# Kernel tuning notes

Measured on AMD Instinct MI355X. Metric: run time of the kernel, lower is better.

Reference implementation:

```python
import jax, jax.numpy as jnp
import numpy as np

N = 50000      # nodes
E = 640000     # edges
HID = 64       # hid_dim (per-head channels C)
HEADS = 4
D = HID * HEADS  # 256, conv output dim (concat=True)
LN_EPS = 1e-5


def setup_inputs() -> dict:
    key = jax.random.key(0)
    ks = jax.random.split(key, 10)
    def w(k, shape, scale=0.05):
        return jax.random.normal(k, shape, dtype=jnp.float32) * scale
    x = jax.random.normal(ks[0], (N, HID), dtype=jnp.float32)
    edge_index = jax.random.randint(ks[1], (2, E), 0, N)
    return {
        'x': x,
        'edge_index': edge_index,
        'Wq': w(ks[2], (D, HID)), 'bq': jnp.zeros((D,), jnp.float32),
        'Wk': w(ks[3], (D, HID)), 'bk': jnp.zeros((D,), jnp.float32),
        'Wv': w(ks[4], (D, HID)), 'bv': jnp.zeros((D,), jnp.float32),
        'Wskip': w(ks[5], (D, HID)), 'bskip': jnp.zeros((D,), jnp.float32),
        'Wbeta': w(ks[6], (1, 3 * D)),
        'ln_g': jnp.ones((D,), jnp.float32), 'ln_b': jnp.zeros((D,), jnp.float32),
        'Wproj': w(ks[7], (HID, D)), 'bproj': jnp.zeros((HID,), jnp.float32),
    }


def _layer(x, edge_index, Wq, bq, Wk, bk, Wv, bv, Wskip, bskip, Wbeta, ln_g, ln_b, Wproj, bproj):
    src, dst = edge_index[0], edge_index[1]  # message flows src -> dst
    # q/k/v projections, [N, H, C]
    q = (x @ Wq.T + bq).reshape(N, HEADS, HID)
    k = (x @ Wk.T + bk).reshape(N, HEADS, HID)
    v = (x @ Wv.T + bv).reshape(N, HEADS, HID)
    # edge-wise attention logits: [E, H]
    alpha = jnp.einsum('ehc,ehc->eh', q[dst], k[src]) / jnp.sqrt(jnp.float32(HID))
    # per-destination-node softmax (segment softmax)
    m = jax.ops.segment_max(alpha, dst, num_segments=N)          # [N, H]
    ex = jnp.exp(alpha - m[dst])                                 # [E, H]
    s = jax.ops.segment_sum(ex, dst, num_segments=N)             # [N, H]
    attn = ex / (s[dst] + 1e-16)                                 # [E, H]
    # weighted scatter-aggregate of values -> [N, H*C]
    msg = (v[src] * attn[..., None]).reshape(E, D)
    out = jax.ops.segment_sum(msg, dst, num_segments=N)          # [N, D]
    # beta gated skip (TransformerConv beta=True, root_weight=True)
    x_r = x @ Wskip.T + bskip                                    # [N, D]
    beta = jax.nn.sigmoid(jnp.concatenate([out, x_r, out - x_r], axis=-1) @ Wbeta.T)  # [N, 1]
    h = beta * x_r + (1.0 - beta) * out
    # LayerNorm over last dim
    mu = jnp.mean(h, axis=-1, keepdims=True)
    var = jnp.var(h, axis=-1, keepdims=True)
    h = (h - mu) * jax.lax.rsqrt(var + LN_EPS) * ln_g + ln_b
    # projection + residual + ReLU (dropout = identity in eval)
    h = h @ Wproj.T + bproj
    return jax.nn.relu(h + x)


def reference(x, edge_index, Wq, bq, Wk, bk, Wv, bv, Wskip, bskip, Wbeta, ln_g, ln_b, Wproj, bproj):
    return _layer(x, edge_index, Wq, bq, Wk, bk, Wv, bv, Wskip, bskip, Wbeta, ln_g, ln_b, Wproj, bproj)
```

## Files before the change

### kernel.cpp

```cpp
#include <hip/hip_runtime.h>
#include <stdint.h>

#define NND 50000
#define NED 640000

typedef unsigned short u16;
typedef unsigned int u32;
typedef __attribute__((ext_vector_type(8))) short short8;
typedef __attribute__((ext_vector_type(4))) float f32x4;
typedef __attribute__((ext_vector_type(2))) float fx2;

__device__ __forceinline__ float bf2f(u16 u) {
    union { u32 i; float f; } x; x.i = ((u32)u) << 16; return x.f;
}
__device__ __forceinline__ u16 f2bf(float f) {
    union { u32 i; float f; } x; x.f = f;
    u32 u = x.i;
    return (u16)((u + 0x7fffu + ((u >> 16) & 1u)) >> 16);
}
__device__ __forceinline__ float bflo(u32 w) {
    union { u32 i; float f; } x; x.i = w << 16; return x.f;
}
__device__ __forceinline__ float bfhi(u32 w) {
    union { u32 i; float f; } x; x.i = w & 0xffff0000u; return x.f;
}
__device__ __forceinline__ u32 pk2(float lo, float hi) {
    return (u32)f2bf(lo) | ((u32)f2bf(hi) << 16);
}
__device__ __forceinline__ u32 pk_fp8_4(u32 w0, u32 w1) {
    u32 p = __builtin_amdgcn_cvt_pk_fp8_f32(bflo(w0), bfhi(w0), 0, false);
    p = __builtin_amdgcn_cvt_pk_fp8_f32(bflo(w1), bfhi(w1), p, true);
    return p;
}
__device__ __forceinline__ void dec8v(u32 a, u32 b, fx2* f) {
    f[0] = __builtin_amdgcn_cvt_pk_f32_fp8(a, false);
    f[1] = __builtin_amdgcn_cvt_pk_f32_fp8(a, true);
    f[2] = __builtin_amdgcn_cvt_pk_f32_fp8(b, false);
    f[3] = __builtin_amdgcn_cvt_pk_f32_fp8(b, true);
}

__global__ void k_wt(const float* __restrict__ Wq, const float* __restrict__ Wk,
                     const float* __restrict__ Wv, const float* __restrict__ Ws,
                     const float* __restrict__ Wp,
                     const float* __restrict__ bq, const float* __restrict__ bk,
                     const float* __restrict__ bv, const float* __restrict__ bs,
                     u16* __restrict__ wb, float* __restrict__ bias_c,
                     u16* __restrict__ wpA) {
    int idx = blockIdx.x * 256 + threadIdx.x;
    if (idx < 65536) {
        int j = idx & 7;
        int lane = (idx >> 3) & 63;
        int q = (idx >> 9) & 1;
        int dt = idx >> 10;
        int dim = dt * 16 + (lane & 15);
        int k = q * 32 + ((lane >> 4) & 3) * 8 + j;
        int mat = dim >> 8, r = dim & 255;
        const float* W = (mat == 0) ? Wq : (mat == 1) ? Wk : (mat == 2) ? Wv : Ws;
        float v = W[r * 64 + k] * ((mat == 0) ? 0.125f : 1.0f);
        wb[idx] = f2bf(v);
    } else if (idx < 65536 + 1024) {
        int dim = idx - 65536;
        int mat = dim >> 8, r = dim & 255;
        const float* B = (mat == 0) ? bq : (mat == 1) ? bk : (mat == 2) ? bv : bs;
        bias_c[dim] = B[r] * ((mat == 0) ? 0.125f : 1.0f);
    } else if (idx < 65536 + 1024 + 16384) {
        int w = idx - 66560;
        int j = w & 7;
        int lane = (w >> 3) & 63;
        int kc = (w >> 9) & 7;
        int mt = w >> 12;
        int dim = mt * 16 + (lane & 15);
        int k = kc * 32 + ((lane >> 4) & 3) * 8 + j;
        wpA[w] = f2bf(Wp[dim * 256 + k]);
    }
}

#define CNT_BLKS 2500
#define PPAD 1040
__global__ __launch_bounds__(256) void k_fillproj(
    const int* __restrict__ esrc, const int* __restrict__ edst,
    int* __restrict__ deg, int* __restrict__ csr,
    const float* __restrict__ x, const u16* __restrict__ wb,
    const float* __restrict__ bias_c,
    uint2* __restrict__ q8, uint4* __restrict__ kv8, u16* __restrict__ xr16)
{
    __shared__ u16 hb[16 * PPAD];
    if (blockIdx.x < CNT_BLKS) {
        int e = blockIdx.x * 256 + threadIdx.x;
        if (e < NED) {
            int d = edst[e];
            int pos = atomicAdd(&deg[d], 1);
            if (pos < 64) csr[(d << 6) + pos] = esrc[e];
        }
        return;
    }
    const int t = threadIdx.x;
    const int wave = t >> 6, lane = t & 63;
    const int node0 = (blockIdx.x - CNT_BLKS) * 16;
    const int lr = lane & 15, quad = lane >> 4;

    int node = node0 + lr;
    if (node > NND - 1) node = NND - 1;
    short8 xf0, xf1;
    {
        const float* xp = x + (size_t)node * 64 + quad * 8;
        float4 a = *reinterpret_cast<const float4*>(xp);
        float4 b = *reinterpret_cast<const float4*>(xp + 4);
        float4 c = *reinterpret_cast<const float4*>(xp + 32);
        float4 d = *reinterpret_cast<const float4*>(xp + 36);
        xf0[0] = (short)f2bf(a.x); xf0[1] = (short)f2bf(a.y);
        xf0[2] = (short)f2bf(a.z); xf0[3] = (short)f2bf(a.w);
        xf0[4] = (short)f2bf(b.x); xf0[5] = (short)f2bf(b.y);
        xf0[6] = (short)f2bf(b.z); xf0[7] = (short)f2bf(b.w);
        xf1[0] = (short)f2bf(c.x); xf1[1] = (short)f2bf(c.y);
        xf1[2] = (short)f2bf(c.z); xf1[3] = (short)f2bf(c.w);
        xf1[4] = (short)f2bf(d.x); xf1[5] = (short)f2bf(d.y);
        xf1[6] = (short)f2bf(d.z); xf1[7] = (short)f2bf(d.w);
    }
    #pragma unroll 4
    for (int dtl = 0; dtl < 16; ++dtl) {
        int dt = wave * 16 + dtl;
        const u16* wp = wb + (size_t)(dt * 2) * 512 + lane * 8;
        short8 a0 = *reinterpret_cast<const short8*>(wp);
        short8 a1 = *reinterpret_cast<const short8*>(wp + 512);
        f32x4 bias = *reinterpret_cast<const f32x4*>(bias_c + dt * 16 + quad * 4);
        f32x4 acc = {0.f, 0.f, 0.f, 0.f};
        acc = __builtin_amdgcn_mfma_f32_16x16x32_bf16(a0, xf0, acc, 0, 0, 0);
        acc = __builtin_amdgcn_mfma_f32_16x16x32_bf16(a1, xf1, acc, 0, 0, 0);
        uint2 st;
        st.x = pk2(acc[0] + bias[0], acc[1] + bias[1]);
        st.y = pk2(acc[2] + bias[2], acc[3] + bias[3]);
        *reinterpret_cast<uint2*>(&hb[lr * PPAD + dt * 16 + quad * 4]) = st;
    }
    __syncthreads();
    #pragma unroll
    for (int it = 0; it < 2; ++it) {
        int idx = it * 256 + t;
        int nip = idx >> 5, g = idx & 31;
        int gnode = node0 + nip;
        if (gnode < NND) {
            const u16* hp = &hb[nip * PPAD];
            *reinterpret_cast<uint4*>(xr16 + (size_t)gnode * 256 + g * 8) =
                *reinterpret_cast<const uint4*>(hp + 768 + g * 8);
            uint4 qw = *reinterpret_cast<const uint4*>(hp + g * 8);
            uint2 qs;
            qs.x = pk_fp8_4(qw.x, qw.y);
            qs.y = pk_fp8_4(qw.z, qw.w);
            q8[(size_t)gnode * 32 + g] = qs;
            uint4 kw = *reinterpret_cast<const uint4*>(hp + 256 + g * 8);
            uint4 vw = *reinterpret_cast<const uint4*>(hp + 512 + g * 8);
            uint4 kvs;
            kvs.x = pk_fp8_4(kw.x, kw.y);
            kvs.y = pk_fp8_4(kw.z, kw.w);
            kvs.z = pk_fp8_4(vw.x, vw.y);
            kvs.w = pk_fp8_4(vw.z, vw.w);
            kv8[(size_t)gnode * 32 + g] = kvs;
        }
    }
}

#define PS 264
__global__ __launch_bounds__(256) void k_attnepi(
    const int* __restrict__ deg, const int* __restrict__ csr,
    const uint2* __restrict__ q8, const uint4* __restrict__ kv8,
    const u16* __restrict__ xr16, const float* __restrict__ x,
    const float* __restrict__ Wbeta, const float* __restrict__ ln_g,
    const float* __restrict__ ln_b, const u16* __restrict__ wpA,
    const float* __restrict__ bproj, float* __restrict__ y)
{
    __shared__ u16 hn[16 * PS];
    const int t = threadIdx.x;
    const int wave = t >> 6, lane = t & 63;
    const int l32 = lane & 31, half = lane >> 5;
    const int lr = lane & 15, grp = lane >> 4;
    const int base = blockIdx.x * 16;

    for (int nt = 0; nt < 4; ++nt) {
        int lid = wave * 4 + nt;
        int node = base + lid;
        if (node >= NND) break;
        uint2 qv = q8[(size_t)node * 32 + l32];
        fx2 q[4];
        dec8v(qv.x, qv.y, q);
        int dg = __builtin_amdgcn_readfirstlane(deg[node]);
        if (dg > 64) dg = 64;
        int r0 = node << 6;
        int r1 = r0 + dg;
        float s = 0.f;
        fx2 acc0 = {0.f, 0.f}, acc1 = {0.f, 0.f}, acc2 = {0.f, 0.f}, acc3 = {0.f, 0.f};
        int i = r0;
        for (; i + 8 <= r1; i += 8) {
            int c0 = csr[i + 0], c1 = csr[i + 1], c2 = csr[i + 2], c3 = csr[i + 3];
            int c4 = csr[i + 4], c5 = csr[i + 5], c6 = csr[i + 6], c7 = csr[i + 7];
            int e0 = half ? c4 : c0;
            int e1 = half ? c5 : c1;
            int e2 = half ? c6 : c2;
            int e3 = half ? c7 : c3;
            uint4 kv0 = kv8[(size_t)e0 * 32 + l32];
            uint4 kv1 = kv8[(size_t)e1 * 32 + l32];
            uint4 kv2 = kv8[(size_t)e2 * 32 + l32];
            uint4 kv3 = kv8[(size_t)e3 * 32 + l32];
            fx2 k0[4], k1[4], k2[4], k3[4];
            dec8v(kv0.x, kv0.y, k0); dec8v(kv1.x, kv1.y, k1);
            dec8v(kv2.x, kv2.y, k2); dec8v(kv3.x, kv3.y, k3);
            fx2 t0 = q[0]*k0[0] + q[1]*k0[1] + q[2]*k0[2] + q[3]*k0[3];
            fx2 t1 = q[0]*k1[0] + q[1]*k1[1] + q[2]*k1[2] + q[3]*k1[3];
            fx2 t2 = q[0]*k2[0] + q[1]*k2[1] + q[2]*k2[2] + q[3]*k2[3];
            fx2 t3 = q[0]*k3[0] + q[1]*k3[1] + q[2]*k3[2] + q[3]*k3[3];
            float pa = t0.x + t0.y, pb = t1.x + t1.y, pc = t2.x + t2.y, pd = t3.x + t3.y;
            pa += __shfl_xor(pa, 1); pa += __shfl_xor(pa, 2); pa += __shfl_xor(pa, 4);
            pb += __shfl_xor(pb, 1); pb += __shfl_xor(pb, 2); pb += __shfl_xor(pb, 4);
            pc += __shfl_xor(pc, 1); pc += __shfl_xor(pc, 2); pc += __shfl_xor(pc, 4);
            pd += __shfl_xor(pd, 1); pd += __shfl_xor(pd, 2); pd += __shfl_xor(pd, 4);
            float ea = __expf(pa), eb = __expf(pb), ec = __expf(pc), ed = __expf(pd);
            s += (ea + eb) + (ec + ed);
            fx2 ev0 = {ea, ea}, ev1 = {eb, eb}, ev2 = {ec, ec}, ev3 = {ed, ed};
            fx2 v0[4], v1[4], v2[4], v3[4];
            dec8v(kv0.z, kv0.w, v0); dec8v(kv1.z, kv1.w, v1);
            dec8v(kv2.z, kv2.w, v2); dec8v(kv3.z, kv3.w, v3);
            acc0 = acc0 + ev0*v0[0] + ev1*v1[0] + ev2*v2[0] + ev3*v3[0];
            acc1 = acc1 + ev0*v0[1] + ev1*v1[1] + ev2*v2[1] + ev3*v3[1];
            acc2 = acc2 + ev0*v0[2] + ev1*v1[2] + ev2*v2[2] + ev3*v3[2];
            acc3 = acc3 + ev0*v0[3] + ev1*v1[3] + ev2*v2[3] + ev3*v3[3];
        }
        for (; i + 4 <= r1; i += 4) {
            int c0 = csr[i + 0], c1 = csr[i + 1], c2 = csr[i + 2], c3 = csr[i + 3];
            int e0 = half ? c2 : c0;
            int e1 = half ? c3 : c1;
            uint4 kv0 = kv8[(size_t)e0 * 32 + l32];
            uint4 kv1 = kv8[(size_t)e1 * 32 + l32];
            fx2 k0[4], k1[4];
            dec8v(kv0.x, kv0.y, k0); dec8v(kv1.x, kv1.y, k1);
            fx2 t0 = q[0]*k0[0] + q[1]*k0[1] + q[2]*k0[2] + q[3]*k0[3];
            fx2 t1 = q[0]*k1[0] + q[1]*k1[1] + q[2]*k1[2] + q[3]*k1[3];
            float pa = t0.x + t0.y, pb = t1.x + t1.y;
            pa += __shfl_xor(pa, 1); pa += __shfl_xor(pa, 2); pa += __shfl_xor(pa, 4);
            pb += __shfl_xor(pb, 1); pb += __shfl_xor(pb, 2); pb += __shfl_xor(pb, 4);
            float ea = __expf(pa), eb = __expf(pb);
            s += ea + eb;
            fx2 ev0 = {ea, ea}, ev1 = {eb, eb};
            fx2 v0[4], v1[4];
            dec8v(kv0.z, kv0.w, v0); dec8v(kv1.z, kv1.w, v1);
            acc0 = acc0 + ev0*v0[0] + ev1*v1[0];
            acc1 = acc1 + ev0*v0[1] + ev1*v1[1];
            acc2 = acc2 + ev0*v0[2] + ev1*v1[2];
            acc3 = acc3 + ev0*v0[3] + ev1*v1[3];
        }
        for (; i < r1; i += 2) {
            int ii = i + half;
            bool valid = ii < r1;
            if (ii > r1 - 1) ii = r1 - 1;
            int e0 = csr[ii];
            uint4 kv0 = kv8[(size_t)e0 * 32 + l32];
            fx2 k0[4];
            dec8v(kv0.x, kv0.y, k0);
            fx2 t0 = q[0]*k0[0] + q[1]*k0[1] + q[2]*k0[2] + q[3]*k0[3];
            float pa = t0.x + t0.y;
            pa += __shfl_xor(pa, 1); pa += __shfl_xor(pa, 2); pa += __shfl_xor(pa, 4);
            float ea = valid ? __expf(pa) : 0.f;
            s += ea;
            fx2 ev0 = {ea, ea};
            fx2 v0[4];
            dec8v(kv0.z, kv0.w, v0);
            acc0 = acc0 + ev0*v0[0];
            acc1 = acc1 + ev0*v0[1];
            acc2 = acc2 + ev0*v0[2];
            acc3 = acc3 + ev0*v0[3];
        }
        float a0 = acc0.x, a1 = acc0.y, a2 = acc1.x, a3 = acc1.y;
        float a4 = acc2.x, a5 = acc2.y, a6 = acc3.x, a7 = acc3.y;
        s  += __shfl_xor(s, 32);
        a0 += __shfl_xor(a0, 32); a1 += __shfl_xor(a1, 32);
        a2 += __shfl_xor(a2, 32); a3 += __shfl_xor(a3, 32);
        a4 += __shfl_xor(a4, 32); a5 += __shfl_xor(a5, 32);
        a6 += __shfl_xor(a6, 32); a7 += __shfl_xor(a7, 32);
        float inv = 1.0f / (s + 1e-16f);
        if (half == 0) {
            uint4 st;
            st.x = pk2(a0 * inv, a1 * inv);
            st.y = pk2(a2 * inv, a3 * inv);
            st.z = pk2(a4 * inv, a5 * inv);
            st.w = pk2(a6 * inv, a7 * inv);
            *reinterpret_cast<uint4*>(&hn[lid * PS + l32 * 8]) = st;
        }
    }
    __syncthreads();

    {
        const float4* wb4 = reinterpret_cast<const float4*>(Wbeta);
        const float4* g44 = reinterpret_cast<const float4*>(ln_g);
        const float4* b44 = reinterpret_cast<const float4*>(ln_b);
        float wo[16], wx[16], wd[16], gg[16], bb[16];
        #pragma unroll
        for (int j = 0; j < 4; ++j) {
            float4 a = wb4[lr * 4 + j];
            float4 b = wb4[64 + lr * 4 + j];
            float4 c = wb4[128 + lr * 4 + j];
            float4 g = g44[lr * 4 + j];
            float4 bl = b44[lr * 4 + j];
            wo[j*4+0]=a.x; wo[j*4+1]=a.y; wo[j*4+2]=a.z; wo[j*4+3]=a.w;
            wx[j*4+0]=b.x; wx[j*4+1]=b.y; wx[j*4+2]=b.z; wx[j*4+3]=b.w;
            wd[j*4+0]=c.x; wd[j*4+1]=c.y; wd[j*4+2]=c.z; wd[j*4+3]=c.w;
            gg[j*4+0]=g.x; gg[j*4+1]=g.y; gg[j*4+2]=g.z; gg[j*4+3]=g.w;
            bb[j*4+0]=bl.x; bb[j*4+1]=bl.y; bb[j*4+2]=bl.z; bb[j*4+3]=bl.w;
        }
        int lid = wave * 4 + grp;
        int node = base + lid;
        if (node < NND) {
            uint4 u0 = *reinterpret_cast<const uint4*>(&hn[lid * PS + lr * 16]);
            uint4 u1 = *reinterpret_cast<const uint4*>(&hn[lid * PS + lr * 16 + 8]);
            const uint4* xp = reinterpret_cast<const uint4*>(xr16 + (size_t)node * 256 + lr * 16);
            uint4 v0 = xp[0], v1 = xp[1];
            float o[16], r[16];
            o[0]=bflo(u0.x); o[1]=bfhi(u0.x); o[2]=bflo(u0.y); o[3]=bfhi(u0.y);
            o[4]=bflo(u0.z); o[5]=bfhi(u0.z); o[6]=bflo(u0.w); o[7]=bfhi(u0.w);
            o[8]=bflo(u1.x); o[9]=bfhi(u1.x); o[10]=bflo(u1.y); o[11]=bfhi(u1.y);
            o[12]=bflo(u1.z); o[13]=bfhi(u1.z); o[14]=bflo(u1.w); o[15]=bfhi(u1.w);
            r[0]=bflo(v0.x); r[1]=bfhi(v0.x); r[2]=bflo(v0.y); r[3]=bfhi(v0.y);
            r[4]=bflo(v0.z); r[5]=bfhi(v0.z); r[6]=bflo(v0.w); r[7]=bfhi(v0.w);
            r[8]=bflo(v1.x); r[9]=bfhi(v1.x); r[10]=bflo(v1.y); r[11]=bfhi(v1.y);
            r[12]=bflo(v1.z); r[13]=bfhi(v1.z); r[14]=bflo(v1.w); r[15]=bfhi(v1.w);
            float part = 0.f;
            #pragma unroll
            for (int cc = 0; cc < 16; ++cc)
                part = fmaf(wo[cc], o[cc], fmaf(wx[cc], r[cc], fmaf(wd[cc], o[cc]-r[cc], part)));
            part += __shfl_xor(part, 1); part += __shfl_xor(part, 2);
            part += __shfl_xor(part, 4); part += __shfl_xor(part, 8);
            float beta = 1.0f / (1.0f + __expf(-part));
            float h[16];
            float sh = 0.f, sq = 0.f;
            #pragma unroll
            for (int cc = 0; cc < 16; ++cc) {
                h[cc] = beta * r[cc] + (1.f - beta) * o[cc];
                sh += h[cc];
                sq = fmaf(h[cc], h[cc], sq);
            }
            sh += __shfl_xor(sh, 1); sh += __shfl_xor(sh, 2);
            sh += __shfl_xor(sh, 4); sh += __shfl_xor(sh, 8);
            sq += __shfl_xor(sq, 1); sq += __shfl_xor(sq, 2);
            sq += __shfl_xor(sq, 4); sq += __shfl_xor(sq, 8);
            float mu = sh * (1.0f / 256.0f);
            float var = sq * (1.0f / 256.0f) - mu * mu;
            float ri = rsqrtf(var + 1e-5f);
            u32 pw[8];
            #pragma unroll
            for (int pp = 0; pp < 8; ++pp) {
                float z0 = (h[pp*2+0] - mu) * ri * gg[pp*2+0] + bb[pp*2+0];
                float z1 = (h[pp*2+1] - mu) * ri * gg[pp*2+1] + bb[pp*2+1];
                pw[pp] = pk2(z0, z1);
            }
            uint4 s0, s1;
            s0.x = pw[0]; s0.y = pw[1]; s0.z = pw[2]; s0.w = pw[3];
            s1.x = pw[4]; s1.y = pw[5]; s1.z = pw[6]; s1.w = pw[7];
            *reinterpret_cast<uint4*>(&hn[lid * PS + lr * 16]) = s0;
            *reinterpret_cast<uint4*>(&hn[lid * PS + lr * 16 + 8]) = s1;
        }
    }
    __syncthreads();

    {
        const int mt = wave;
        f32x4 acc = {0.f, 0.f, 0.f, 0.f};
        #pragma unroll
        for (int kc = 0; kc < 8; ++kc) {
            short8 a = *reinterpret_cast<const short8*>(wpA + ((size_t)(mt * 8 + kc) * 64 + lane) * 8);
            short8 b = *reinterpret_cast<const short8*>(&hn[lr * PS + kc * 32 + grp * 8]);
            acc = __builtin_amdgcn_mfma_f32_16x16x32_bf16(a, b, acc, 0, 0, 0);
        }
        int node = base + lr;
        if (node < NND) {
            int d0 = mt * 16 + grp * 4;
            float4 bp4 = *reinterpret_cast<const float4*>(bproj + d0);
            float4 xv = *reinterpret_cast<const float4*>(x + (size_t)node * 64 + d0);
            float4 rr;
            rr.x = fmaxf(acc[0] + bp4.x + xv.x, 0.f);
            rr.y = fmaxf(acc[1] + bp4.y + xv.y, 0.f);
            rr.z = fmaxf(acc[2] + bp4.z + xv.z, 0.f);
            rr.w = fmaxf(acc[3] + bp4.w + xv.w, 0.f);
            *reinterpret_cast<float4*>(y + (size_t)node * 64 + d0) = rr;
        }
    }
}

extern "C" void kernel_launch(void* const* d_in, const int* in_sizes, int n_in,
                              void* d_out, int out_size, void* d_ws, size_t ws_size,
                              hipStream_t stream) {
    const float* x     = (const float*)d_in[0];
    const int*   eidx  = (const int*)d_in[1];
    const float* Wq    = (const float*)d_in[2];
    const float* bq    = (const float*)d_in[3];
    const float* Wk    = (const float*)d_in[4];
    const float* bk    = (const float*)d_in[5];
    const float* Wv    = (const float*)d_in[6];
    const float* bv    = (const float*)d_in[7];
    const float* Wsk   = (const float*)d_in[8];
    const float* bsk   = (const float*)d_in[9];
    const float* Wbeta = (const float*)d_in[10];
    const float* lng   = (const float*)d_in[11];
    const float* lnb   = (const float*)d_in[12];
    const float* Wp    = (const float*)d_in[13];
    const float* bp    = (const float*)d_in[14];
    float* y = (float*)d_out;

    char* ws = (char*)d_ws;
    size_t off = 0;
    auto alloc = [&](size_t b) { size_t o = off; off += (b + 255) & ~(size_t)255; return o; };
    uint2* q8   = (uint2*)(ws + alloc((size_t)NND * 256));
    uint4* kv8  = (uint4*)(ws + alloc((size_t)NND * 512));
    u16*  xr16  = (u16*)(ws + alloc((size_t)NND * 512));
    int* deg    = (int*)(ws + alloc((size_t)NND * 4));
    int* csr    = (int*)(ws + alloc((size_t)NND * 64 * 4));
    u16* wb     = (u16*)(ws + alloc((size_t)65536 * 2));
    float* bias_c = (float*)(ws + alloc((size_t)1024 * 4));
    u16* wpA    = (u16*)(ws + alloc((size_t)16384 * 2));

    hipMemsetAsync(deg, 0, (size_t)NND * 4, stream);
    k_wt      <<<324, 256, 0, stream>>>(Wq, Wk, Wv, Wsk, Wp, bq, bk, bv, bsk,
                                        wb, bias_c, wpA);
    k_fillproj<<<CNT_BLKS + (NND + 15) / 16, 256, 0, stream>>>(
                 eidx, eidx + NED, deg, csr, x, wb, bias_c, q8, kv8, xr16);
    k_attnepi <<<(NND + 15) / 16, 256, 0, stream>>>(deg, csr, q8, kv8, xr16, x,
                                                    Wbeta, lng, lnb, wpA, bp, y);
}
```

Before: 238.4 us.

## Prefetch kv gathers, vectorize csr loads, 32 nodes per block, fold deg memset

The attention kernel now software-pipelines its gather loop: it loads the next 8 neighbours' CSR indices (as int4) and kv rows before processing the current batch, so memory latency overlaps compute. Each block handles 32 nodes instead of 16, and the epilogue and MFMA projection loop twice per wave, which spreads weight loads over more nodes. The deg memset moves into the weight-prep kernel, removing one launch. The prefetch registers and larger LDS footprint raise register and shared-memory pressure, which may reduce occupancy.

New measurement: 241.4 us. Within noise of the previous version (+1.2%).

```diff
diff --git a/kernel.cpp b/kernel.cpp
--- a/kernel.cpp
+++ b/kernel.cpp
@@ -45,7 +45,7 @@
                      const float* __restrict__ bq, const float* __restrict__ bk,
                      const float* __restrict__ bv, const float* __restrict__ bs,
                      u16* __restrict__ wb, float* __restrict__ bias_c,
-                     u16* __restrict__ wpA) {
+                     u16* __restrict__ wpA, int* __restrict__ deg) {
     int idx = blockIdx.x * 256 + threadIdx.x;
     if (idx < 65536) {
         int j = idx & 7;
@@ -72,6 +72,8 @@
         int dim = mt * 16 + (lane & 15);
         int k = kc * 32 + ((lane >> 4) & 3) * 8 + j;
         wpA[w] = f2bf(Wp[dim * 256 + k]);
+    } else if (idx < 65536 + 1024 + 16384 + NND) {
+        deg[idx - 82944] = 0;
     }
 }
 
@@ -160,6 +162,7 @@
 }
 
 #define PS 264
+#define NPB 32
 __global__ __launch_bounds__(256) void k_attnepi(
     const int* __restrict__ deg, const int* __restrict__ csr,
     const uint2* __restrict__ q8, const uint4* __restrict__ kv8,
@@ -168,15 +171,16 @@
     const float* __restrict__ ln_b, const u16* __restrict__ wpA,
     const float* __restrict__ bproj, float* __restrict__ y)
 {
-    __shared__ u16 hn[16 * PS];
+    __shared__ u16 hn[NPB * PS];
     const int t = threadIdx.x;
-    const int wave = t >> 6, lane = t & 63;
+    const int wave = __builtin_amdgcn_readfirstlane(t >> 6);
+    const int lane = t & 63;
     const int l32 = lane & 31, half = lane >> 5;
     const int lr = lane & 15, grp = lane >> 4;
-    const int base = blockIdx.x * 16;
-
-    for (int nt = 0; nt < 4; ++nt) {
-        int lid = wave * 4 + nt;
+    const int base = blockIdx.x * NPB;
+
+    for (int nt = 0; nt < 8; ++nt) {
+        int lid = wave * 8 + nt;
         int node = base + lid;
         if (node >= NND) break;
         uint2 qv = q8[(size_t)node * 32 + l32];
@@ -188,21 +192,11 @@
         int r1 = r0 + dg;
         float s = 0.f;
         fx2 acc0 = {0.f, 0.f}, acc1 = {0.f, 0.f}, acc2 = {0.f, 0.f}, acc3 = {0.f, 0.f};
-        int i = r0;
-        for (; i + 8 <= r1; i += 8) {
-            int c0 = csr[i + 0], c1 = csr[i + 1], c2 = csr[i + 2], c3 = csr[i + 3];
-            int c4 = csr[i + 4], c5 = csr[i + 5], c6 = csr[i + 6], c7 = csr[i + 7];
-            int e0 = half ? c4 : c0;
-            int e1 = half ? c5 : c1;
-            int e2 = half ? c6 : c2;
-            int e3 = half ? c7 : c3;
-            uint4 kv0 = kv8[(size_t)e0 * 32 + l32];
-            uint4 kv1 = kv8[(size_t)e1 * 32 + l32];
-            uint4 kv2 = kv8[(size_t)e2 * 32 + l32];
-            uint4 kv3 = kv8[(size_t)e3 * 32 + l32];
+
+        auto proc4 = [&](uint4 kva, uint4 kvb, uint4 kvc, uint4 kvd) {
             fx2 k0[4], k1[4], k2[4], k3[4];
-            dec8v(kv0.x, kv0.y, k0); dec8v(kv1.x, kv1.y, k1);
-            dec8v(kv2.x, kv2.y, k2); dec8v(kv3.x, kv3.y, k3);
+            dec8v(kva.x, kva.y, k0); dec8v(kvb.x, kvb.y, k1);
+            dec8v(kvc.x, kvc.y, k2); dec8v(kvd.x, kvd.y, k3);
             fx2 t0 = q[0]*k0[0] + q[1]*k0[1] + q[2]*k0[2] + q[3]*k0[3];
             fx2 t1 = q[0]*k1[0] + q[1]*k1[1] + q[2]*k1[2] + q[3]*k1[3];
             fx2 t2 = q[0]*k2[0] + q[1]*k2[1] + q[2]*k2[2] + q[3]*k2[3];
@@ -216,12 +210,44 @@
             s += (ea + eb) + (ec + ed);
             fx2 ev0 = {ea, ea}, ev1 = {eb, eb}, ev2 = {ec, ec}, ev3 = {ed, ed};
             fx2 v0[4], v1[4], v2[4], v3[4];
-            dec8v(kv0.z, kv0.w, v0); dec8v(kv1.z, kv1.w, v1);
-            dec8v(kv2.z, kv2.w, v2); dec8v(kv3.z, kv3.w, v3);
+            dec8v(kva.z, kva.w, v0); dec8v(kvb.z, kvb.w, v1);
+            dec8v(kvc.z, kvc.w, v2); dec8v(kvd.z, kvd.w, v3);
             acc0 = acc0 + ev0*v0[0] + ev1*v1[0] + ev2*v2[0] + ev3*v3[0];
             acc1 = acc1 + ev0*v0[1] + ev1*v1[1] + ev2*v2[1] + ev3*v3[1];
             acc2 = acc2 + ev0*v0[2] + ev1*v1[2] + ev2*v2[2] + ev3*v3[2];
             acc3 = acc3 + ev0*v0[3] + ev1*v1[3] + ev2*v2[3] + ev3*v3[3];
+        };
+
+        int i = r0;
+        int nfull = (r1 - r0) >> 3;
+        if (nfull > 0) {
+            int4 ca = *reinterpret_cast<const int4*>(csr + i);
+            int4 cb = *reinterpret_cast<const int4*>(csr + i + 4);
+            int e0 = half ? cb.x : ca.x;
+            int e1 = half ? cb.y : ca.y;
+            int e2 = half ? cb.z : ca.z;
+            int e3 = half ? cb.w : ca.w;
+            uint4 kv0 = kv8[(size_t)e0 * 32 + l32];
+            uint4 kv1 = kv8[(size_t)e1 * 32 + l32];
+            uint4 kv2 = kv8[(size_t)e2 * 32 + l32];
+            uint4 kv3 = kv8[(size_t)e3 * 32 + l32];
+            for (int b = 1; b < nfull; ++b) {
+                i += 8;
+                int4 na = *reinterpret_cast<const int4*>(csr + i);
+                int4 nb = *reinterpret_cast<const int4*>(csr + i + 4);
+                int f0 = half ? nb.x : na.x;
+                int f1 = half ? nb.y : na.y;
+                int f2 = half ? nb.z : na.z;
+                int f3 = half ? nb.w : na.w;
+                uint4 n0 = kv8[(size_t)f0 * 32 + l32];
+                uint4 n1 = kv8[(size_t)f1 * 32 + l32];
+                uint4 n2 = kv8[(size_t)f2 * 32 + l32];
+                uint4 n3 = kv8[(size_t)f3 * 32 + l32];
+                proc4(kv0, kv1, kv2, kv3);
+                kv0 = n0; kv1 = n1; kv2 = n2; kv3 = n3;
+            }
+            proc4(kv0, kv1, kv2, kv3);
+            i += 8;
         }
         for (; i + 4 <= r1; i += 4) {
             int c0 = csr[i + 0], c1 = csr[i + 1], c2 = csr[i + 2], c3 = csr[i + 3];
@@ -304,80 +330,86 @@
             gg[j*4+0]=g.x; gg[j*4+1]=g.y; gg[j*4+2]=g.z; gg[j*4+3]=g.w;
             bb[j*4+0]=bl.x; bb[j*4+1]=bl.y; bb[j*4+2]=bl.z; bb[j*4+3]=bl.w;
         }
-        int lid = wave * 4 + grp;
-        int node = base + lid;
-        if (node < NND) {
-            uint4 u0 = *reinterpret_cast<const uint4*>(&hn[lid * PS + lr * 16]);
-            uint4 u1 = *reinterpret_cast<const uint4*>(&hn[lid * PS + lr * 16 + 8]);
-            const uint4* xp = reinterpret_cast<const uint4*>(xr16 + (size_t)node * 256 + lr * 16);
-            uint4 v0 = xp[0], v1 = xp[1];
-            float o[16], r[16];
-            o[0]=bflo(u0.x); o[1]=bfhi(u0.x); o[2]=bflo(u0.y); o[3]=bfhi(u0.y);
-            o[4]=bflo(u0.z); o[5]=bfhi(u0.z); o[6]=bflo(u0.w); o[7]=bfhi(u0.w);
-            o[8]=bflo(u1.x); o[9]=bfhi(u1.x); o[10]=bflo(u1.y); o[11]=bfhi(u1.y);
-            o[12]=bflo(u1.z); o[13]=bfhi(u1.z); o[14]=bflo(u1.w); o[15]=bfhi(u1.w);
-            r[0]=bflo(v0.x); r[1]=bfhi(v0.x); r[2]=bflo(v0.y); r[3]=bfhi(v0.y);
-            r[4]=bflo(v0.z); r[5]=bfhi(v0.z); r[6]=bflo(v0.w); r[7]=bfhi(v0.w);
-            r[8]=bflo(v1.x); r[9]=bfhi(v1.x); r[10]=bflo(v1.y); r[11]=bfhi(v1.y);
-            r[12]=bflo(v1.z); r[13]=bfhi(v1.z); r[14]=bflo(v1.w); r[15]=bfhi(v1.w);
-            float part = 0.f;
-            #pragma unroll
-            for (int cc = 0; cc < 16; ++cc)
-                part = fmaf(wo[cc], o[cc], fmaf(wx[cc], r[cc], fmaf(wd[cc], o[cc]-r[cc], part)));
-            part += __shfl_xor(part, 1); part += __shfl_xor(part, 2);
-            part += __shfl_xor(part, 4); part += __shfl_xor(part, 8);
-            float beta = 1.0f / (1.0f + __expf(-part));
-            float h[16];
-            float sh = 0.f, sq = 0.f;
-            #pragma unroll
-            for (int cc = 0; cc < 16; ++cc) {
-                h[cc] = beta * r[cc] + (1.f - beta) * o[cc];
-                sh += h[cc];
-                sq = fmaf(h[cc], h[cc], sq);
+        #pragma unroll
+        for (int p = 0; p < 2; ++p) {
+            int lid = p * 16 + wave * 4 + grp;
+            int node = base + lid;
+            if (node < NND) {
+                uint4 u0 = *reinterpret_cast<const uint4*>(&hn[lid * PS + lr * 16]);
+                uint4 u1 = *reinterpret_cast<const uint4*>(&hn[lid * PS + lr * 16 + 8]);
+                const uint4* xp = reinterpret_cast<const uint4*>(xr16 + (size_t)node * 256 + lr * 16);
+                uint4 v0 = xp[0], v1 = xp[1];
+                float o[16], r[16];
+                o[0]=bflo(u0.x); o[1]=bfhi(u0.x); o[2]=bflo(u0.y); o[3]=bfhi(u0.y);
+                o[4]=bflo(u0.z); o[5]=bfhi(u0.z); o[6]=bflo(u0.w); o[7]=bfhi(u0.w);
+                o[8]=bflo(u1.x); o[9]=bfhi(u1.x); o[10]=bflo(u1.y); o[11]=bfhi(u1.y);
+                o[12]=bflo(u1.z); o[13]=bfhi(u1.z); o[14]=bflo(u1.w); o[15]=bfhi(u1.w);
+                r[0]=bflo(v0.x); r[1]=bfhi(v0.x); r[2]=bflo(v0.y); r[3]=bfhi(v0.y);
+                r[4]=bflo(v0.z); r[5]=bfhi(v0.z); r[6]=bflo(v0.w); r[7]=bfhi(v0.w);
+                r[8]=bflo(v1.x); r[9]=bfhi(v1.x); r[10]=bflo(v1.y); r[11]=bfhi(v1.y);
+                r[12]=bflo(v1.z); r[13]=bfhi(v1.z); r[14]=bflo(v1.w); r[15]=bfhi(v1.w);
+                float part = 0.f;
+                #pragma unroll
+                for (int cc = 0; cc < 16; ++cc)
+                    part = fmaf(wo[cc], o[cc], fmaf(wx[cc], r[cc], fmaf(wd[cc], o[cc]-r[cc], part)));
+                part += __shfl_xor(part, 1); part += __shfl_xor(part, 2);
+                part += __shfl_xor(part, 4); part += __shfl_xor(part, 8);
+                float beta = 1.0f / (1.0f + __expf(-part));
+                float h[16];
+                float sh = 0.f, sq = 0.f;
+                #pragma unroll
+                for (int cc = 0; cc < 16; ++cc) {
+                    h[cc] = beta * r[cc] + (1.f - beta) * o[cc];
+                    sh += h[cc];
+                    sq = fmaf(h[cc], h[cc], sq);
+                }
+                sh += __shfl_xor(sh, 1); sh += __shfl_xor(sh, 2);
+                sh += __shfl_xor(sh, 4); sh += __shfl_xor(sh, 8);
+                sq += __shfl_xor(sq, 1); sq += __shfl_xor(sq, 2);
+                sq += __shfl_xor(sq, 4); sq += __shfl_xor(sq, 8);
+                float mu = sh * (1.0f / 256.0f);
+                float var = sq * (1.0f / 256.0f) - mu * mu;
+                float ri = rsqrtf(var + 1e-5f);
+                u32 pw[8];
+                #pragma unroll
+                for (int pp = 0; pp < 8; ++pp) {
+                    float z0 = (h[pp*2+0] - mu) * ri * gg[pp*2+0] + bb[pp*2+0];
+                    float z1 = (h[pp*2+1] - mu) * ri * gg[pp*2+1] + bb[pp*2+1];
+                    pw[pp] = pk2(z0, z1);
+                }
+                uint4 s0, s1;
+                s0.x = pw[0]; s0.y = pw[1]; s0.z = pw[2]; s0.w = pw[3];
+                s1.x = pw[4]; s1.y = pw[5]; s1.z = pw[6]; s1.w = pw[7];
+                *reinterpret_cast<uint4*>(&hn[lid * PS + lr * 16]) = s0;
+                *reinterpret_cast<uint4*>(&hn[lid * PS + lr * 16 + 8]) = s1;
             }
-            sh += __shfl_xor(sh, 1); sh += __shfl_xor(sh, 2);
-            sh += __shfl_xor(sh, 4); sh += __shfl_xor(sh, 8);
-            sq += __shfl_xor(sq, 1); sq += __shfl_xor(sq, 2);
-            sq += __shfl_xor(sq, 4); sq += __shfl_xor(sq, 8);
-            float mu = sh * (1.0f / 256.0f);
-            float var = sq * (1.0f / 256.0f) - mu * mu;
-            float ri = rsqrtf(var + 1e-5f);
-            u32 pw[8];
-            #pragma unroll
-            for (int pp = 0; pp < 8; ++pp) {
-                float z0 = (h[pp*2+0] - mu) * ri * gg[pp*2+0] + bb[pp*2+0];
-                float z1 = (h[pp*2+1] - mu) * ri * gg[pp*2+1] + bb[pp*2+1];
-                pw[pp] = pk2(z0, z1);
-            }
-            uint4 s0, s1;
-            s0.x = pw[0]; s0.y = pw[1]; s0.z = pw[2]; s0.w = pw[3];
-            s1.x = pw[4]; s1.y = pw[5]; s1.z = pw[6]; s1.w = pw[7];
-            *reinterpret_cast<uint4*>(&hn[lid * PS + lr * 16]) = s0;
-            *reinterpret_cast<uint4*>(&hn[lid * PS + lr * 16 + 8]) = s1;
         }
     }
     __syncthreads();
 
     {
         const int mt = wave;
-        f32x4 acc = {0.f, 0.f, 0.f, 0.f};
         #pragma unroll
-        for (int kc = 0; kc < 8; ++kc) {
-            short8 a = *reinterpret_cast<const short8*>(wpA + ((size_t)(mt * 8 + kc) * 64 + lane) * 8);
-            short8 b = *reinterpret_cast<const short8*>(&hn[lr * PS + kc * 32 + grp * 8]);
-            acc = __builtin_amdgcn_mfma_f32_16x16x32_bf16(a, b, acc, 0, 0, 0);
-        }
-        int node = base + lr;
-        if (node < NND) {
-            int d0 = mt * 16 + grp * 4;
-            float4 bp4 = *reinterpret_cast<const float4*>(bproj + d0);
-            float4 xv = *reinterpret_cast<const float4*>(x + (size_t)node * 64 + d0);
-            float4 rr;
-            rr.x = fmaxf(acc[0] + bp4.x + xv.x, 0.f);
-            rr.y = fmaxf(acc[1] + bp4.y + xv.y, 0.f);
-            rr.z = fmaxf(acc[2] + bp4.z + xv.z, 0.f);
-            rr.w = fmaxf(acc[3] + bp4.w + xv.w, 0.f);
-            *reinterpret_cast<float4*>(y + (size_t)node * 64 + d0) = rr;
+        for (int p = 0; p < 2; ++p) {
+            f32x4 acc = {0.f, 0.f, 0.f, 0.f};
+            #pragma unroll
+            for (int kc = 0; kc < 8; ++kc) {
+                short8 a = *reinterpret_cast<const short8*>(wpA + ((size_t)(mt * 8 + kc) * 64 + lane) * 8);
+                short8 b = *reinterpret_cast<const short8*>(&hn[(p * 16 + lr) * PS + kc * 32 + grp * 8]);
+                acc = __builtin_amdgcn_mfma_f32_16x16x32_bf16(a, b, acc, 0, 0, 0);
+            }
+            int node = base + p * 16 + lr;
+            if (node < NND) {
+                int d0 = mt * 16 + grp * 4;
+                float4 bp4 = *reinterpret_cast<const float4*>(bproj + d0);
+                float4 xv = *reinterpret_cast<const float4*>(x + (size_t)node * 64 + d0);
+                float4 rr;
+                rr.x = fmaxf(acc[0] + bp4.x + xv.x, 0.f);
+                rr.y = fmaxf(acc[1] + bp4.y + xv.y, 0.f);
+                rr.z = fmaxf(acc[2] + bp4.z + xv.z, 0.f);
+                rr.w = fmaxf(acc[3] + bp4.w + xv.w, 0.f);
+                *reinterpret_cast<float4*>(y + (size_t)node * 64 + d0) = rr;
+            }
         }
     }
 }
@@ -414,11 +446,10 @@
     float* bias_c = (float*)(ws + alloc((size_t)1024 * 4));
     u16* wpA    = (u16*)(ws + alloc((size_t)16384 * 2));
 
-    hipMemsetAsync(deg, 0, (size_t)NND * 4, stream);
-    k_wt      <<<324, 256, 0, stream>>>(Wq, Wk, Wv, Wsk, Wp, bq, bk, bv, bsk,
-                                        wb, bias_c, wpA);
+    k_wt      <<<520, 256, 0, stream>>>(Wq, Wk, Wv, Wsk, Wp, bq, bk, bv, bsk,
+                                        wb, bias_c, wpA, deg);
     k_fillproj<<<CNT_BLKS + (NND + 15) / 16, 256, 0, stream>>>(
                  eidx, eidx + NED, deg, csr, x, wb, bias_c, q8, kv8, xr16);
-    k_attnepi <<<(NND + 15) / 16, 256, 0, stream>>>(deg, csr, q8, kv8, xr16, x,
-                                                    Wbeta, lng, lnb, wpA, bp, y);
-}
+    k_attnepi <<<(NND + NPB - 1) / NPB, 256, 0, stream>>>(deg, csr, q8, kv8, xr16, x,
+                                                          Wbeta, lng, lnb, wpA, bp, y);
+}
```
